# Kernel tuning notes

Hardware: AMD Instinct MI355X
Metric: run time of the kernel (lower is better)

## Reference

```python
import jax, jax.numpy as jnp
import numpy as np

N = 100000    # nodes
E = 800000    # directed edges
EF = 16       # edge features
NF = 1        # node features (forced by the module's MLP-size constraint)
HID = NF * 8  # NNConv out = 8
H1, C1 = 8, 16  # gat1 heads / per-head channels -> 128
NC = 16       # num_classes (gat2: heads=1, out=NC)


def setup_inputs() -> dict:
    key = jax.random.key(0)
    ks = jax.random.split(key, 20)
    s = 0.1
    return {
        "x": jax.random.normal(ks[0], (N, NF), jnp.float32),
        "edge_index": jax.random.randint(ks[1], (2, E), 0, N, jnp.int64),
        "edge_attr": jax.random.normal(ks[2], (E, EF), jnp.float32),
        # edge MLP: Linear(EF,8) -> ReLU -> Linear(8,8)
        "w1": jax.random.normal(ks[3], (EF, HID), jnp.float32) * s,
        "b1": jnp.zeros((HID,), jnp.float32),
        "w2": jax.random.normal(ks[4], (HID, HID), jnp.float32) * s,
        "b2": jnp.zeros((HID,), jnp.float32),
        # NNConv root weight + bias
        "root": jax.random.normal(ks[5], (NF, HID), jnp.float32) * s,
        "nn_bias": jnp.zeros((HID,), jnp.float32),
        # GAT1: in 8 -> 16 ch x 8 heads
        "g1W": jax.random.normal(ks[6], (HID, H1 * C1), jnp.float32) * s,
        "g1as": jax.random.normal(ks[7], (H1, C1), jnp.float32) * s,
        "g1ad": jax.random.normal(ks[8], (H1, C1), jnp.float32) * s,
        "g1b": jnp.zeros((H1 * C1,), jnp.float32),
        # GAT2: in 128 -> NC, 1 head
        "g2W": jax.random.normal(ks[9], (H1 * C1, NC), jnp.float32) * s,
        "g2as": jax.random.normal(ks[10], (1, NC), jnp.float32) * s,
        "g2ad": jax.random.normal(ks[11], (1, NC), jnp.float32) * s,
        "g2b": jnp.zeros((NC,), jnp.float32),
    }


def _gat(h_in, W, a_src, a_dst, bias, src, dst, n, heads, ch):
    # h: [N, heads, ch]
    h = (h_in @ W).reshape(n, heads, ch)
    e_s = jnp.einsum("nhc,hc->nh", h, a_src)   # per-node src logits
    e_d = jnp.einsum("nhc,hc->nh", h, a_dst)
    e = jax.nn.leaky_relu(e_s[src] + e_d[dst], 0.2)      # [E2, heads]
    m = jax.ops.segment_max(e, dst, num_segments=n)      # segment softmax
    e = jnp.exp(e - m[dst])
    z = jax.ops.segment_sum(e, dst, num_segments=n)
    alpha = e / (z[dst] + 1e-16)                          # [E2, heads]
    out = jax.ops.segment_sum(alpha[:, :, None] * h[src], dst, num_segments=n)
    return out.reshape(n, heads * ch) + bias


def reference(x, edge_index, edge_attr, w1, b1, w2, b2, root, nn_bias,
              g1W, g1as, g1ad, g1b, g2W, g2as, g2ad, g2b):
    n = x.shape[0]
    src, dst = edge_index[0], edge_index[1]

    # ---- NNConv (aggr='mean'): per-edge weight from edge MLP ----
    w_e = jax.nn.relu(edge_attr @ w1 + b1) @ w2 + b2      # [E, NF*HID]
    w_e = w_e.reshape(-1, NF, HID)
    msg = jnp.einsum("ei,eio->eo", x[src], w_e)            # [E, HID]
    sums = jax.ops.segment_sum(msg, dst, num_segments=n)
    cnt = jax.ops.segment_sum(jnp.ones((msg.shape[0],), msg.dtype), dst, num_segments=n)
    aggr = sums / jnp.maximum(cnt, 1.0)[:, None]
    h = jax.nn.relu(aggr + x @ root + nn_bias)             # [N, 8]
    # dropout: eval mode -> identity

    # ---- add self-loops (PyG GATConv default) ----
    loops = jnp.arange(n, dtype=src.dtype)
    src2 = jnp.concatenate([src, loops])
    dst2 = jnp.concatenate([dst, loops])

    h = jax.nn.elu(_gat(h, g1W, g1as, g1ad, g1b, src2, dst2, n, H1, C1))  # [N,128]
    out = _gat(h, g2W, g2as, g2ad, g2b, src2, dst2, n, 1, NC)             # [N,16]
    return jax.nn.log_softmax(out, axis=1)
```

## Files before the change

### kernel.cpp

```cpp
#include <hip/hip_runtime.h>
#include <hip/hip_fp16.h>
#include <math.h>

constexpr int NN  = 100000;
constexpr int NE  = 800000;
constexpr int H1 = 8, C1 = 16;
constexpr int D1 = H1 * C1;
constexpr int NC = 16;
constexpr int CAP = 40;
constexpr float LOG2E = 1.44269504f;
constexpr float MSC   = 32.f;

static inline int cdiv(int a, int b) { return (a + b - 1) / b; }

typedef int   v4i __attribute__((ext_vector_type(4)));
typedef float v2f __attribute__((ext_vector_type(2)));

__device__ inline __half2 h2_bits(unsigned u) {
    __half2 r; __builtin_memcpy(&r, &u, 4); return r;
}
__device__ inline __half2 shflx_h2(__half2 v, int off) {
    int iv; __builtin_memcpy(&iv, &v, 4);
    iv = __shfl_xor(iv, off);
    __half2 r; __builtin_memcpy(&r, &iv, 4); return r;
}

__global__ void fill_cur(int* __restrict__ cur) {
    int i = blockIdx.x * blockDim.x + threadIdx.x;
    if (i < NN) cur[i] = i * CAP;
}

__global__ void nnconv_scatter(const float* __restrict__ x,
                               const int* __restrict__ src, const int* __restrict__ dst,
                               const float* __restrict__ ea,
                               const float* __restrict__ w1, const float* __restrict__ b1,
                               const float* __restrict__ w2, const float* __restrict__ b2,
                               int* __restrict__ cursor,
                               int* __restrict__ rec_s) {
    __shared__ float sw1[16 * 8], sw2[8 * 8], sb1[8], sb2[8];
    int t = threadIdx.x;
    if (t < 128) sw1[t] = w1[t];
    else if (t < 192) sw2[t - 128] = w2[t - 128];
    else if (t < 200) sb1[t - 192] = b1[t - 192];
    else if (t < 208) sb2[t - 200] = b2[t - 200];
    __syncthreads();
    int e = blockIdx.x * blockDim.x + t;
    if (e >= NE) return;

    float a[16];
    const float4* ea4 = (const float4*)(ea + (size_t)e * 16);
    float4 v0 = ea4[0], v1 = ea4[1], v2 = ea4[2], v3 = ea4[3];
    a[0]=v0.x; a[1]=v0.y; a[2]=v0.z; a[3]=v0.w;
    a[4]=v1.x; a[5]=v1.y; a[6]=v1.z; a[7]=v1.w;
    a[8]=v2.x; a[9]=v2.y; a[10]=v2.z; a[11]=v2.w;
    a[12]=v3.x; a[13]=v3.y; a[14]=v3.z; a[15]=v3.w;

    float hdn[8];
#pragma unroll
    for (int j = 0; j < 8; j++) {
        float s = sb1[j];
#pragma unroll
        for (int i = 0; i < 16; i++) s = fmaf(a[i], sw1[i * 8 + j], s);
        hdn[j] = fmaxf(s, 0.f);
    }
    int sn = src[e], dn = dst[e];
    float xv = x[sn] * MSC;
    float m[8];
#pragma unroll
    for (int j = 0; j < 8; j++) {
        float s = sb2[j];
#pragma unroll
        for (int i = 0; i < 8; i++) s = fmaf(hdn[i], sw2[i * 8 + j], s);
        m[j] = xv * s;
    }
    int wa = __builtin_amdgcn_cvt_pk_fp8_f32(m[0], m[1], 0, false);
    wa     = __builtin_amdgcn_cvt_pk_fp8_f32(m[2], m[3], wa, true);
    int wb = __builtin_amdgcn_cvt_pk_fp8_f32(m[4], m[5], 0, false);
    wb     = __builtin_amdgcn_cvt_pk_fp8_f32(m[6], m[7], wb, true);

    int pos = atomicAdd(&cursor[dn], 1);
    if (pos < dn * CAP + CAP) {
        v4i rec; rec[0] = sn; rec[1] = wa; rec[2] = wb; rec[3] = 0;
        __builtin_nontemporal_store(rec, (v4i*)(rec_s + (size_t)pos * 4));
    }
}

__global__ void fused_node1(const float* __restrict__ x,
                            const int* __restrict__ cur,
                            const int* __restrict__ rec_s,
                            const float* __restrict__ root, const float* __restrict__ nb,
                            const float* __restrict__ W,
                            const float* __restrict__ as_, const float* __restrict__ ad_,
                            unsigned char* __restrict__ h1f8,
                            float* __restrict__ es, float* __restrict__ ed) {
    int t = blockIdx.x * blockDim.x + threadIdx.x;
    if (t >= NN * 8) return;
    int n = t >> 3, j = t & 7;
    int rs = n * CAP;
    int d = min(cur[n] - rs, CAP);

    v2f pp0 = {0.f, 0.f}, pp1 = {0.f, 0.f}, pp2 = {0.f, 0.f}, pp3 = {0.f, 0.f};
    for (int k = j; k < d; k += 8) {
        uint4 m = *(const uint4*)(rec_s + (size_t)(rs + k) * 4);
        pp0 += __builtin_amdgcn_cvt_pk_f32_fp8(m.y, false);
        pp1 += __builtin_amdgcn_cvt_pk_f32_fp8(m.y, true);
        pp2 += __builtin_amdgcn_cvt_pk_f32_fp8(m.z, false);
        pp3 += __builtin_amdgcn_cvt_pk_f32_fp8(m.z, true);
    }
    float p0 = pp0[0], p1 = pp0[1], p2 = pp1[0], p3 = pp1[1];
    float p4 = pp2[0], p5 = pp2[1], p6 = pp3[0], p7 = pp3[1];
    float k0 = (j & 4) ? p4 : p0, s0 = (j & 4) ? p0 : p4;
    float k1 = (j & 4) ? p5 : p1, s1 = (j & 4) ? p1 : p5;
    float k2 = (j & 4) ? p6 : p2, s2 = (j & 4) ? p2 : p6;
    float k3 = (j & 4) ? p7 : p3, s3 = (j & 4) ? p3 : p7;
    k0 += __shfl_xor(s0, 4); k1 += __shfl_xor(s1, 4);
    k2 += __shfl_xor(s2, 4); k3 += __shfl_xor(s3, 4);
    float m0 = (j & 2) ? k2 : k0, n0 = (j & 2) ? k0 : k2;
    float m1 = (j & 2) ? k3 : k1, n1 = (j & 2) ? k1 : k3;
    m0 += __shfl_xor(n0, 2); m1 += __shfl_xor(n1, 2);
    float q  = (j & 1) ? m1 : m0, r = (j & 1) ? m0 : m1;
    float sum = q + __shfl_xor(r, 1);

    float inv = 1.f / (MSC * fmaxf((float)d, 1.f));
    float hj = fmaxf(fmaf(sum, inv, x[n] * root[j] + nb[j]), 0.f);

    float hv[8];
#pragma unroll
    for (int k = 0; k < 8; k++) hv[k] = __shfl(hj, k, 8);

    int hd = j;
    v2f aa0 = {0.f,0.f}, aa1 = {0.f,0.f}, aa2 = {0.f,0.f}, aa3 = {0.f,0.f};
    v2f aa4 = {0.f,0.f}, aa5 = {0.f,0.f}, aa6 = {0.f,0.f}, aa7 = {0.f,0.f};
#define ACCK(hk, kk) do { const float4* w4_ = (const float4*)(W + (kk) * D1 + hd * 16); \
        float4 u0 = w4_[0], u1 = w4_[1], u2 = w4_[2], u3 = w4_[3]; \
        v2f h2_; h2_[0] = hk; h2_[1] = hk; v2f t_; \
        t_[0]=u0.x; t_[1]=u0.y; aa0 = __builtin_elementwise_fma(h2_, t_, aa0); \
        t_[0]=u0.z; t_[1]=u0.w; aa1 = __builtin_elementwise_fma(h2_, t_, aa1); \
        t_[0]=u1.x; t_[1]=u1.y; aa2 = __builtin_elementwise_fma(h2_, t_, aa2); \
        t_[0]=u1.z; t_[1]=u1.w; aa3 = __builtin_elementwise_fma(h2_, t_, aa3); \
        t_[0]=u2.x; t_[1]=u2.y; aa4 = __builtin_elementwise_fma(h2_, t_, aa4); \
        t_[0]=u2.z; t_[1]=u2.w; aa5 = __builtin_elementwise_fma(h2_, t_, aa5); \
        t_[0]=u3.x; t_[1]=u3.y; aa6 = __builtin_elementwise_fma(h2_, t_, aa6); \
        t_[0]=u3.z; t_[1]=u3.w; aa7 = __builtin_elementwise_fma(h2_, t_, aa7); } while (0)
    ACCK(hv[0], 0); ACCK(hv[1], 1); ACCK(hv[2], 2); ACCK(hv[3], 3);
    ACCK(hv[4], 4); ACCK(hv[5], 5); ACCK(hv[6], 6); ACCK(hv[7], 7);
#undef ACCK

    const float4* as4 = (const float4*)(as_ + hd * 16);
    const float4* ad4 = (const float4*)(ad_ + hd * 16);
    v2f sv2 = {0.f, 0.f}, dv2 = {0.f, 0.f};
    { float4 u;
      u = as4[0]; v2f t; t[0]=u.x; t[1]=u.y; sv2 = __builtin_elementwise_fma(aa0, t, sv2);
                  t[0]=u.z; t[1]=u.w; sv2 = __builtin_elementwise_fma(aa1, t, sv2);
      u = as4[1]; t[0]=u.x; t[1]=u.y; sv2 = __builtin_elementwise_fma(aa2, t, sv2);
                  t[0]=u.z; t[1]=u.w; sv2 = __builtin_elementwise_fma(aa3, t, sv2);
      u = as4[2]; t[0]=u.x; t[1]=u.y; sv2 = __builtin_elementwise_fma(aa4, t, sv2);
                  t[0]=u.z; t[1]=u.w; sv2 = __builtin_elementwise_fma(aa5, t, sv2);
      u = as4[3]; t[0]=u.x; t[1]=u.y; sv2 = __builtin_elementwise_fma(aa6, t, sv2);
                  t[0]=u.z; t[1]=u.w; sv2 = __builtin_elementwise_fma(aa7, t, sv2);
      u = ad4[0]; t[0]=u.x; t[1]=u.y; dv2 = __builtin_elementwise_fma(aa0, t, dv2);
                  t[0]=u.z; t[1]=u.w; dv2 = __builtin_elementwise_fma(aa1, t, dv2);
      u = ad4[1]; t[0]=u.x; t[1]=u.y; dv2 = __builtin_elementwise_fma(aa2, t, dv2);
                  t[0]=u.z; t[1]=u.w; dv2 = __builtin_elementwise_fma(aa3, t, dv2);
      u = ad4[2]; t[0]=u.x; t[1]=u.y; dv2 = __builtin_elementwise_fma(aa4, t, dv2);
                  t[0]=u.z; t[1]=u.w; dv2 = __builtin_elementwise_fma(aa5, t, dv2);
      u = ad4[3]; t[0]=u.x; t[1]=u.y; dv2 = __builtin_elementwise_fma(aa6, t, dv2);
                  t[0]=u.z; t[1]=u.w; dv2 = __builtin_elementwise_fma(aa7, t, dv2);
    }
    float sv = sv2[0] + sv2[1], dv = dv2[0] + dv2[1];

    v4i pk;
    int wd;
    wd = __builtin_amdgcn_cvt_pk_fp8_f32(aa0[0] * 16.f, aa0[1] * 16.f, 0, false);
    wd = __builtin_amdgcn_cvt_pk_fp8_f32(aa1[0] * 16.f, aa1[1] * 16.f, wd, true);
    pk[0] = wd;
    wd = __builtin_amdgcn_cvt_pk_fp8_f32(aa2[0] * 16.f, aa2[1] * 16.f, 0, false);
    wd = __builtin_amdgcn_cvt_pk_fp8_f32(aa3[0] * 16.f, aa3[1] * 16.f, wd, true);
    pk[1] = wd;
    wd = __builtin_amdgcn_cvt_pk_fp8_f32(aa4[0] * 16.f, aa4[1] * 16.f, 0, false);
    wd = __builtin_amdgcn_cvt_pk_fp8_f32(aa5[0] * 16.f, aa5[1] * 16.f, wd, true);
    pk[2] = wd;
    wd = __builtin_amdgcn_cvt_pk_fp8_f32(aa6[0] * 16.f, aa6[1] * 16.f, 0, false);
    wd = __builtin_amdgcn_cvt_pk_fp8_f32(aa7[0] * 16.f, aa7[1] * 16.f, wd, true);
    pk[3] = wd;
    *(v4i*)(h1f8 + (unsigned)n * 128u + hd * 16) = pk;
    es[t] = sv * LOG2E;
    ed[t] = dv * LOG2E;
}

__global__ __launch_bounds__(256) void gat1_gather(
        const int* __restrict__ cur,
        const int* __restrict__ rec_s,
        const float* __restrict__ es, const float* __restrict__ ed,
        const unsigned char* __restrict__ h1f8, const float* __restrict__ b,
        const float* __restrict__ W2,
        const float* __restrict__ as2, const float* __restrict__ ad2,
        __half* __restrict__ h2h, float* __restrict__ es2, float* __restrict__ ed2) {
    __shared__ float sW2t[16 * 130];
    __shared__ float so[4][4][132];
    int tid = threadIdx.x;
    for (int idx = tid; idx < 2048; idx += 256)
        sW2t[(idx & 15) * 130 + (idx >> 4)] = W2[idx];
    __syncthreads();

    int wv = tid >> 6, lane = tid & 63;
    int g  = lane >> 4;
    int cl = lane & 15;
    int hd = cl >> 1;
    float4 bv0 = *((const float4*)(b + cl * 8));
    float4 bv1 = *((const float4*)(b + cl * 8 + 4));

    int base = (blockIdx.x * 4 + wv) * 4;
    for (int i = 0; i < 4; i++) {
        int node = base + i;
        int rs = node * CAP;
        int d = min(cur[node] - rs, CAP);
        const int* sp = rec_s + (size_t)rs * 4;
        float edn = ed[(unsigned)node * 8u + hd];

        float vs = es[(unsigned)node * 8u + hd] + edn;
        vs = fmaxf(vs, 0.2f * vs);
        float a0 = (g == 0) ? __builtin_amdgcn_exp2f(vs) : 0.f;
        float z = a0;
        uint2 gl = *(const uint2*)(h1f8 + (unsigned)node * 128u + cl * 8);
        v2f a02; a02[0] = a0; a02[1] = a0;
        v2f c01 = a02 * __builtin_amdgcn_cvt_pk_f32_fp8(gl.x, false);
        v2f c23 = a02 * __builtin_amdgcn_cvt_pk_f32_fp8(gl.x, true);
        v2f c45 = a02 * __builtin_amdgcn_cvt_pk_f32_fp8(gl.y, false);
        v2f c67 = a02 * __builtin_amdgcn_cvt_pk_f32_fp8(gl.y, true);

        for (int k = g; k < d; k += 8) {
            int s0 = sp[k << 2];
            int k2 = k + 4;
            bool pair = k2 < d;
            int s1 = pair ? sp[k2 << 2] : s0;
            float v0 = es[(unsigned)s0 * 8u + hd] + edn;
            float v1 = es[(unsigned)s1 * 8u + hd] + edn;
            v0 = fmaxf(v0, 0.2f * v0);
            v1 = fmaxf(v1, 0.2f * v1);
            float aA = __builtin_amdgcn_exp2f(v0);
            float aB = pair ? __builtin_amdgcn_exp2f(v1) : 0.f;
            uint2 geA = *(const uint2*)(h1f8 + (unsigned)s0 * 128u + cl * 8);
            uint2 geB = *(const uint2*)(h1f8 + (unsigned)s1 * 128u + cl * 8);
            z += aA + aB;
            v2f a2A; a2A[0] = aA; a2A[1] = aA;
            v2f a2B; a2B[0] = aB; a2B[1] = aB;
            c01 = __builtin_elementwise_fma(a2A, __builtin_amdgcn_cvt_pk_f32_fp8(geA.x, false), c01);
            c23 = __builtin_elementwise_fma(a2A, __builtin_amdgcn_cvt_pk_f32_fp8(geA.x, true),  c23);
            c45 = __builtin_elementwise_fma(a2A, __builtin_amdgcn_cvt_pk_f32_fp8(geA.y, false), c45);
            c67 = __builtin_elementwise_fma(a2A, __builtin_amdgcn_cvt_pk_f32_fp8(geA.y, true),  c67);
            c01 = __builtin_elementwise_fma(a2B, __builtin_amdgcn_cvt_pk_f32_fp8(geB.x, false), c01);
            c23 = __builtin_elementwise_fma(a2B, __builtin_amdgcn_cvt_pk_f32_fp8(geB.x, true),  c23);
            c45 = __builtin_elementwise_fma(a2B, __builtin_amdgcn_cvt_pk_f32_fp8(geB.y, false), c45);
            c67 = __builtin_elementwise_fma(a2B, __builtin_amdgcn_cvt_pk_f32_fp8(geB.y, true),  c67);
        }
        z += __shfl_xor(z, 16); z += __shfl_xor(z, 32);
#define RED(cc) do { \
        cc[0] += __shfl_xor(cc[0], 16); cc[0] += __shfl_xor(cc[0], 32); \
        cc[1] += __shfl_xor(cc[1], 16); cc[1] += __shfl_xor(cc[1], 32); } while (0)
        RED(c01); RED(c23); RED(c45); RED(c67);
#undef RED

        float rz = 1.f / (16.f * (z + 1e-16f));
        float o0 = fmaf(c01[0], rz, bv0.x), o1 = fmaf(c01[1], rz, bv0.y);
        float o2 = fmaf(c23[0], rz, bv0.z), o3 = fmaf(c23[1], rz, bv0.w);
        float o4 = fmaf(c45[0], rz, bv1.x), o5 = fmaf(c45[1], rz, bv1.y);
        float o6 = fmaf(c67[0], rz, bv1.z), o7 = fmaf(c67[1], rz, bv1.w);
        o0 = o0 > 0.f ? o0 : __expf(o0) - 1.f;
        o1 = o1 > 0.f ? o1 : __expf(o1) - 1.f;
        o2 = o2 > 0.f ? o2 : __expf(o2) - 1.f;
        o3 = o3 > 0.f ? o3 : __expf(o3) - 1.f;
        o4 = o4 > 0.f ? o4 : __expf(o4) - 1.f;
        o5 = o5 > 0.f ? o5 : __expf(o5) - 1.f;
        o6 = o6 > 0.f ? o6 : __expf(o6) - 1.f;
        o7 = o7 > 0.f ? o7 : __expf(o7) - 1.f;
        if (g == 0) {
            float4* sp2 = (float4*)&so[wv][i][cl * 8];
            sp2[0] = make_float4(o0, o1, o2, o3);
            sp2[1] = make_float4(o4, o5, o6, o7);
        }
    }
    __asm__ __volatile__("s_waitcnt lgkmcnt(0)" ::: "memory");

    int nl = lane >> 4, c = lane & 15;
    const float* wt = sW2t + c * 130;
    v2f part = {0.f, 0.f};
#pragma unroll 8
    for (int k = 0; k < 128; k += 2) {
        float2 sv = *(const float2*)&so[wv][nl][k];
        v2f sv2; sv2[0] = sv.x; sv2[1] = sv.y;
        v2f wv2 = *(const v2f*)&wt[k];
        part = __builtin_elementwise_fma(sv2, wv2, part);
    }
    float partial = part[0] + part[1];
    float ta = partial * as2[c], tb = partial * ad2[c];
#pragma unroll
    for (int off = 1; off < 16; off <<= 1) {
        ta += __shfl_xor(ta, off);
        tb += __shfl_xor(tb, off);
    }
    h2h[(unsigned)(base + nl) * 16u + c] = __float2half(partial);
    if (c == 0) {
        es2[base + nl] = ta * LOG2E;
        ed2[base + nl] = tb * LOG2E;
    }
}

__global__ __launch_bounds__(256) void gat2_gather(
        const int* __restrict__ cur,
        const int* __restrict__ rec_s,
        const float* __restrict__ es, const float* __restrict__ ed,
        const __half* __restrict__ h2h, const float* __restrict__ b,
        float* __restrict__ out) {
    int tid = threadIdx.x;
    int wv = tid >> 6, lane = tid & 63;
    int g = lane >> 3, l = lane & 7;
    const unsigned* h2i = (const unsigned*)h2h;
    float2 bv = ((const float2*)b)[l];
    int base = (blockIdx.x * 4 + wv) * 4;
    for (int i = 0; i < 4; i++) {
        int node = base + i;
        int rs = node * CAP;
        int d = min(cur[node] - rs, CAP);
        const int* sp = rec_s + (size_t)rs * 4;
        float edn = ed[node];
        float vs = es[node] + edn;
        vs = fmaxf(vs, 0.2f * vs);
        float a0 = (g == 0) ? __builtin_amdgcn_exp2f(vs) : 0.f;
        float z = a0;
        __half2 acc = __hmul2(__float2half2_rn(a0),
                              h2_bits(h2i[(unsigned)node * 8u + l]));

        for (int k = g; k < d; k += 8) {
            int s = sp[k << 2];
            float v = es[s] + edn;
            v = fmaxf(v, 0.2f * v);
            float a = __builtin_amdgcn_exp2f(v);
            unsigned hraw = h2i[(unsigned)s * 8u + l];
            z += a;
            acc = __hfma2(__float2half2_rn(a), h2_bits(hraw), acc);
        }
        z += __shfl_xor(z, 8); z += __shfl_xor(z, 16); z += __shfl_xor(z, 32);
        acc = __hadd2(acc, shflx_h2(acc, 8));
        acc = __hadd2(acc, shflx_h2(acc, 16));
        acc = __hadd2(acc, shflx_h2(acc, 32));

        float rz = 1.f / (z + 1e-16f);
        float2 f = __half22float2(acc);
        float o0 = fmaf(f.x, rz, bv.x);
        float o1 = fmaf(f.y, rz, bv.y);
        float mx = fmaxf(o0, o1);
        mx = fmaxf(mx, __shfl_xor(mx, 1));
        mx = fmaxf(mx, __shfl_xor(mx, 2));
        mx = fmaxf(mx, __shfl_xor(mx, 4));
        float ss = __expf(o0 - mx) + __expf(o1 - mx);
        ss += __shfl_xor(ss, 1); ss += __shfl_xor(ss, 2); ss += __shfl_xor(ss, 4);
        float lg = mx + __logf(ss);
        if (g == 0)
            ((float2*)out)[(unsigned)node * 8u + l] = make_float2(o0 - lg, o1 - lg);
    }
}

extern "C" void kernel_launch(void* const* d_in, const int* in_sizes, int n_in,
                              void* d_out, int out_size, void* d_ws, size_t ws_size,
                              hipStream_t stream) {
    const float* x    = (const float*)d_in[0];
    const int*   ei   = (const int*)d_in[1];
    const float* ea   = (const float*)d_in[2];
    const float* w1   = (const float*)d_in[3];
    const float* b1   = (const float*)d_in[4];
    const float* w2   = (const float*)d_in[5];
    const float* b2   = (const float*)d_in[6];
    const float* root = (const float*)d_in[7];
    const float* nb   = (const float*)d_in[8];
    const float* g1W  = (const float*)d_in[9];
    const float* g1as = (const float*)d_in[10];
    const float* g1ad = (const float*)d_in[11];
    const float* g1b  = (const float*)d_in[12];
    const float* g2W  = (const float*)d_in[13];
    const float* g2as = (const float*)d_in[14];
    const float* g2ad = (const float*)d_in[15];
    const float* g2b  = (const float*)d_in[16];
    float* out = (float*)d_out;

    const int* src = ei;
    const int* dst = ei + NE;

    float* ws = (float*)d_ws;
    size_t o = 0;
    int* rec_s = (int*)(ws + o); o += (size_t)NN * CAP * 4;
    unsigned char* h1f8 = (unsigned char*)(ws + o); o += (size_t)NN * 32;
    __half* h2h    = (__half*)(ws + o); o += (size_t)NN * NC / 2;
    int*  cur   = (int*)(ws + o); o += NN;
    float* es1  = ws + o; o += (size_t)NN * H1;
    float* ed1  = ws + o; o += (size_t)NN * H1;
    float* es2  = ws + o; o += NN;
    float* ed2  = ws + o; o += NN;
    (void)ws_size; (void)in_sizes; (void)n_in; (void)out_size;

    const int B = 256;

    fill_cur<<<cdiv(NN, B), B, 0, stream>>>(cur);

    nnconv_scatter<<<cdiv(NE, B), B, 0, stream>>>(x, src, dst, ea, w1, b1, w2, b2,
                                                  cur, rec_s);
    fused_node1<<<cdiv(NN * 8, B), B, 0, stream>>>(x, cur, rec_s, root, nb,
                                                   g1W, g1as, g1ad, h1f8, es1, ed1);
    gat1_gather<<<NN / 16, B, 0, stream>>>(cur, rec_s, es1, ed1, h1f8,
                                           g1b, g2W, g2as, g2ad, h2h, es2, ed2);
    gat2_gather<<<NN / 16, B, 0, stream>>>(cur, rec_s, es2, ed2, h2h, g2b, out);
}
```

Measured before the change: 292.6 us.

## Aggregate NNConv messages with float atomics and shrink CSR records to source indices

NNConv messages are no longer packed as fp8 into 16-byte per-edge records and reduced later in fused_node1. Each edge now atomically adds its 8 float messages into a zeroed per-node aggregate buffer, and stores only the source index in a compact 4-byte CSR slot. This cuts record write and read traffic for all three gather stages, gives denser index reads in the GAT gathers, and removes the fp8 quantisation of messages. The cost is eight float atomics per edge plus a zeroing pass.

After: 586.9 us. +100.6%, slower.

```diff
diff --git a/kernel.cpp b/kernel.cpp
--- a/kernel.cpp
+++ b/kernel.cpp
@@ -9,7 +9,6 @@
 constexpr int NC = 16;
 constexpr int CAP = 40;
 constexpr float LOG2E = 1.44269504f;
-constexpr float MSC   = 32.f;
 
 static inline int cdiv(int a, int b) { return (a + b - 1) / b; }
 
@@ -25,9 +24,14 @@
     __half2 r; __builtin_memcpy(&r, &iv, 4); return r;
 }
 
-__global__ void fill_cur(int* __restrict__ cur) {
+__global__ void fill_cur(int* __restrict__ cur, float* __restrict__ aggr) {
     int i = blockIdx.x * blockDim.x + threadIdx.x;
-    if (i < NN) cur[i] = i * CAP;
+    if (i < NN) {
+        cur[i] = i * CAP;
+        uint4 z = {0u, 0u, 0u, 0u};
+        ((uint4*)aggr)[i * 2]     = z;
+        ((uint4*)aggr)[i * 2 + 1] = z;
+    }
 }
 
 __global__ void nnconv_scatter(const float* __restrict__ x,
@@ -36,7 +40,7 @@
                                const float* __restrict__ w1, const float* __restrict__ b1,
                                const float* __restrict__ w2, const float* __restrict__ b2,
                                int* __restrict__ cursor,
-                               int* __restrict__ rec_s) {
+                               int* __restrict__ src_s, float* __restrict__ aggr) {
     __shared__ float sw1[16 * 8], sw2[8 * 8], sb1[8], sb2[8];
     int t = threadIdx.x;
     if (t < 128) sw1[t] = w1[t];
@@ -55,6 +59,10 @@
     a[8]=v2.x; a[9]=v2.y; a[10]=v2.z; a[11]=v2.w;
     a[12]=v3.x; a[13]=v3.y; a[14]=v3.z; a[15]=v3.w;
 
+    int sn = src[e], dn = dst[e];
+    int pos = atomicAdd(&cursor[dn], 1);
+    float xv = x[sn];
+
     float hdn[8];
 #pragma unroll
     for (int j = 0; j < 8; j++) {
@@ -63,31 +71,21 @@
         for (int i = 0; i < 16; i++) s = fmaf(a[i], sw1[i * 8 + j], s);
         hdn[j] = fmaxf(s, 0.f);
     }
-    int sn = src[e], dn = dst[e];
-    float xv = x[sn] * MSC;
-    float m[8];
+    float* ag = aggr + (size_t)dn * 8;
 #pragma unroll
     for (int j = 0; j < 8; j++) {
         float s = sb2[j];
 #pragma unroll
         for (int i = 0; i < 8; i++) s = fmaf(hdn[i], sw2[i * 8 + j], s);
-        m[j] = xv * s;
-    }
-    int wa = __builtin_amdgcn_cvt_pk_fp8_f32(m[0], m[1], 0, false);
-    wa     = __builtin_amdgcn_cvt_pk_fp8_f32(m[2], m[3], wa, true);
-    int wb = __builtin_amdgcn_cvt_pk_fp8_f32(m[4], m[5], 0, false);
-    wb     = __builtin_amdgcn_cvt_pk_fp8_f32(m[6], m[7], wb, true);
-
-    int pos = atomicAdd(&cursor[dn], 1);
-    if (pos < dn * CAP + CAP) {
-        v4i rec; rec[0] = sn; rec[1] = wa; rec[2] = wb; rec[3] = 0;
-        __builtin_nontemporal_store(rec, (v4i*)(rec_s + (size_t)pos * 4));
-    }
+        unsafeAtomicAdd(ag + j, xv * s);
+    }
+    if (pos < dn * CAP + CAP)
+        src_s[pos] = sn;
 }
 
 __global__ void fused_node1(const float* __restrict__ x,
                             const int* __restrict__ cur,
-                            const int* __restrict__ rec_s,
+                            const float* __restrict__ aggr,
                             const float* __restrict__ root, const float* __restrict__ nb,
                             const float* __restrict__ W,
                             const float* __restrict__ as_, const float* __restrict__ ad_,
@@ -96,33 +94,10 @@
     int t = blockIdx.x * blockDim.x + threadIdx.x;
     if (t >= NN * 8) return;
     int n = t >> 3, j = t & 7;
-    int rs = n * CAP;
-    int d = min(cur[n] - rs, CAP);
-
-    v2f pp0 = {0.f, 0.f}, pp1 = {0.f, 0.f}, pp2 = {0.f, 0.f}, pp3 = {0.f, 0.f};
-    for (int k = j; k < d; k += 8) {
-        uint4 m = *(const uint4*)(rec_s + (size_t)(rs + k) * 4);
-        pp0 += __builtin_amdgcn_cvt_pk_f32_fp8(m.y, false);
-        pp1 += __builtin_amdgcn_cvt_pk_f32_fp8(m.y, true);
-        pp2 += __builtin_amdgcn_cvt_pk_f32_fp8(m.z, false);
-        pp3 += __builtin_amdgcn_cvt_pk_f32_fp8(m.z, true);
-    }
-    float p0 = pp0[0], p1 = pp0[1], p2 = pp1[0], p3 = pp1[1];
-    float p4 = pp2[0], p5 = pp2[1], p6 = pp3[0], p7 = pp3[1];
-    float k0 = (j & 4) ? p4 : p0, s0 = (j & 4) ? p0 : p4;
-    float k1 = (j & 4) ? p5 : p1, s1 = (j & 4) ? p1 : p5;
-    float k2 = (j & 4) ? p6 : p2, s2 = (j & 4) ? p2 : p6;
-    float k3 = (j & 4) ? p7 : p3, s3 = (j & 4) ? p3 : p7;
-    k0 += __shfl_xor(s0, 4); k1 += __shfl_xor(s1, 4);
-    k2 += __shfl_xor(s2, 4); k3 += __shfl_xor(s3, 4);
-    float m0 = (j & 2) ? k2 : k0, n0 = (j & 2) ? k0 : k2;
-    float m1 = (j & 2) ? k3 : k1, n1 = (j & 2) ? k1 : k3;
-    m0 += __shfl_xor(n0, 2); m1 += __shfl_xor(n1, 2);
-    float q  = (j & 1) ? m1 : m0, r = (j & 1) ? m0 : m1;
-    float sum = q + __shfl_xor(r, 1);
-
-    float inv = 1.f / (MSC * fmaxf((float)d, 1.f));
-    float hj = fmaxf(fmaf(sum, inv, x[n] * root[j] + nb[j]), 0.f);
+    int d = min(cur[n] - n * CAP, CAP);
+
+    float sum = aggr[t];
+    float hj = fmaxf(sum / fmaxf((float)d, 1.f) + x[n] * root[j] + nb[j], 0.f);
 
     float hv[8];
 #pragma unroll
@@ -190,7 +165,7 @@
 
 __global__ __launch_bounds__(256) void gat1_gather(
         const int* __restrict__ cur,
-        const int* __restrict__ rec_s,
+        const int* __restrict__ src_s,
         const float* __restrict__ es, const float* __restrict__ ed,
         const unsigned char* __restrict__ h1f8, const float* __restrict__ b,
         const float* __restrict__ W2,
@@ -215,7 +190,7 @@
         int node = base + i;
         int rs = node * CAP;
         int d = min(cur[node] - rs, CAP);
-        const int* sp = rec_s + (size_t)rs * 4;
+        const int* sp = src_s + rs;
         float edn = ed[(unsigned)node * 8u + hd];
 
         float vs = es[(unsigned)node * 8u + hd] + edn;
@@ -230,10 +205,10 @@
         v2f c67 = a02 * __builtin_amdgcn_cvt_pk_f32_fp8(gl.y, true);
 
         for (int k = g; k < d; k += 8) {
-            int s0 = sp[k << 2];
+            int s0 = sp[k];
             int k2 = k + 4;
             bool pair = k2 < d;
-            int s1 = pair ? sp[k2 << 2] : s0;
+            int s1 = pair ? sp[k2] : s0;
             float v0 = es[(unsigned)s0 * 8u + hd] + edn;
             float v1 = es[(unsigned)s1 * 8u + hd] + edn;
             v0 = fmaxf(v0, 0.2f * v0);
@@ -308,7 +283,7 @@
 
 __global__ __launch_bounds__(256) void gat2_gather(
         const int* __restrict__ cur,
-        const int* __restrict__ rec_s,
+        const int* __restrict__ src_s,
         const float* __restrict__ es, const float* __restrict__ ed,
         const __half* __restrict__ h2h, const float* __restrict__ b,
         float* __restrict__ out) {
@@ -322,7 +297,7 @@
         int node = base + i;
         int rs = node * CAP;
         int d = min(cur[node] - rs, CAP);
-        const int* sp = rec_s + (size_t)rs * 4;
+        const int* sp = src_s + rs;
         float edn = ed[node];
         float vs = es[node] + edn;
         vs = fmaxf(vs, 0.2f * vs);
@@ -332,7 +307,7 @@
                               h2_bits(h2i[(unsigned)node * 8u + l]));
 
         for (int k = g; k < d; k += 8) {
-            int s = sp[k << 2];
+            int s = sp[k];
             float v = es[s] + edn;
             v = fmaxf(v, 0.2f * v);
             float a = __builtin_amdgcn_exp2f(v);
@@ -388,7 +363,8 @@
 
     float* ws = (float*)d_ws;
     size_t o = 0;
-    int* rec_s = (int*)(ws + o); o += (size_t)NN * CAP * 4;
+    int*  src_s = (int*)(ws + o); o += (size_t)NN * CAP;
+    float* aggr = ws + o; o += (size_t)NN * 8;
     unsigned char* h1f8 = (unsigned char*)(ws + o); o += (size_t)NN * 32;
     __half* h2h    = (__half*)(ws + o); o += (size_t)NN * NC / 2;
     int*  cur   = (int*)(ws + o); o += NN;
@@ -400,13 +376,13 @@
 
     const int B = 256;
 
-    fill_cur<<<cdiv(NN, B), B, 0, stream>>>(cur);
+    fill_cur<<<cdiv(NN, B), B, 0, stream>>>(cur, aggr);
 
     nnconv_scatter<<<cdiv(NE, B), B, 0, stream>>>(x, src, dst, ea, w1, b1, w2, b2,
-                                                  cur, rec_s);
-    fused_node1<<<cdiv(NN * 8, B), B, 0, stream>>>(x, cur, rec_s, root, nb,
+                                                  cur, src_s, aggr);
+    fused_node1<<<cdiv(NN * 8, B), B, 0, stream>>>(x, cur, aggr, root, nb,
                                                    g1W, g1as, g1ad, h1f8, es1, ed1);
-    gat1_gather<<<NN / 16, B, 0, stream>>>(cur, rec_s, es1, ed1, h1f8,
+    gat1_gather<<<NN / 16, B, 0, stream>>>(cur, src_s, es1, ed1, h1f8,
                                            g1b, g2W, g2as, g2ad, h2h, es2, ed2);
-    gat2_gather<<<NN / 16, B, 0, stream>>>(cur, rec_s, es2, ed2, h2h, g2b, out);
-}
+    gat2_gather<<<NN / 16, B, 0, stream>>>(cur, src_s, es2, ed2, h2h, g2b, out);
+}
```
